# Kernel tuning notes

Measured on AMD Instinct MI355X. Metric: run time of the kernel, lower is better.

The kernel has to match this reference:

```python
import jax, jax.numpy as jnp
import numpy as np

B, S, D, H = 4, 2048, 1024, 16
DEPTH = D // H
NEG = -1000000000.0


def setup_inputs() -> dict:
    key = jax.random.key(0)
    ks = jax.random.split(key, 11)
    scale = 1.0 / np.sqrt(D)
    return {
        "q": jax.random.normal(ks[0], (B, S, D), jnp.float32),
        "k": jax.random.normal(ks[1], (B, S, D), jnp.float32),
        "v": jax.random.normal(ks[2], (B, S, D), jnp.float32),
        "wq_w": jax.random.normal(ks[3], (D, D), jnp.float32) * scale,
        "wq_b": jax.random.normal(ks[4], (D,), jnp.float32) * 0.01,
        "wk_w": jax.random.normal(ks[5], (D, D), jnp.float32) * scale,
        "wk_b": jax.random.normal(ks[6], (D,), jnp.float32) * 0.01,
        "wv_w": jax.random.normal(ks[7], (D, D), jnp.float32) * scale,
        "wv_b": jax.random.normal(ks[8], (D,), jnp.float32) * 0.01,
        "dense_w": jax.random.normal(ks[9], (D, D), jnp.float32) * scale,
        "dense_b": jax.random.normal(ks[10], (D,), jnp.float32) * 0.01,
    }


def _split_heads(x):
    # (B, S, D) -> (B, H, S, depth)
    b, s, _ = x.shape
    return x.reshape(b, s, H, DEPTH).transpose(0, 2, 1, 3)


def reference(q, k, v, wq_w, wq_b, wk_w, wk_b, wv_w, wv_b, dense_w, dense_b):
    b, s, _ = q.shape
    qh = _split_heads(q @ wq_w.T + wq_b)
    kh = _split_heads(k @ wk_w.T + wk_b)
    vh = _split_heads(v @ wv_w.T + wv_b)
    logits = jnp.einsum('bhqd,bhkd->bhqk', qh, kh) / np.sqrt(DEPTH).astype(np.float32)
    # additive causal mask (strict upper triangle = -1e9)
    mask = jnp.where(jnp.triu(jnp.ones((s, s), jnp.float32), k=1) == 1.0, NEG, 0.0)
    logits = logits + mask
    attn = jax.nn.softmax(logits, axis=-1)
    out = jnp.einsum('bhqk,bhkd->bhqd', attn, vh)
    out = out.transpose(0, 2, 1, 3).reshape(b, s, D)
    return out @ dense_w.T + dense_b
```

## Files before the change

### kernel.cpp

```cpp
#include <hip/hip_runtime.h>
#include <hip/hip_bf16.h>


typedef __attribute__((ext_vector_type(8))) short bf16x8;
typedef __attribute__((ext_vector_type(4))) float f32x4;
typedef __attribute__((ext_vector_type(8))) unsigned short u16x8;

#define MFMA16(a, b, c) __builtin_amdgcn_mfma_f32_16x16x32_bf16(a, b, c, 0, 0, 0)

#define GLOAD_LDS16(gp, lp)                                                    \
  __builtin_amdgcn_global_load_lds(                                            \
      (const __attribute__((address_space(1))) void*)(gp),                     \
      (__attribute__((address_space(3))) void*)(lp), 16, 0, 0)

__device__ __forceinline__ unsigned short f2bf(float f) {
  union { float f; unsigned u; } x; x.f = f;
  unsigned u = x.u;
  return (unsigned short)((u + 0x7fffu + ((u >> 16) & 1u)) >> 16);
}

__device__ __forceinline__ unsigned pk2(float a, float b) {
  union { __hip_bfloat162 h; unsigned u; } cv;
  cv.h = __float22bfloat162_rn(float2{a, b});
  return cv.u;
}

__global__ __launch_bounds__(256) void convert_kernel(
    const float* __restrict__ q, const float* __restrict__ k,
    const float* __restrict__ v, const float* __restrict__ wq,
    const float* __restrict__ wk, const float* __restrict__ wv,
    const float* __restrict__ wd, const float* __restrict__ bq,
    const float* __restrict__ bk, const float* __restrict__ bv,
    unsigned short* __restrict__ dst, float* __restrict__ bias_pack) {
  const size_t tid0 = (size_t)blockIdx.x * blockDim.x + threadIdx.x;
  const size_t nthreads = (size_t)gridDim.x * blockDim.x;
  if (tid0 < 3072) {
    bias_pack[tid0] = tid0 < 1024 ? bq[tid0]
                     : (tid0 < 2048 ? bk[tid0 - 1024] : bv[tid0 - 2048]);
  }
  const size_t NQ = 8192ull * 1024;
  const size_t NW = 1024ull * 1024;
  const size_t total_chunks = (3 * NQ + 4 * NW) / 8;
  for (size_t c = tid0; c < total_chunks; c += nthreads) {
    const size_t e = c * 8;
    const float* src;
    if (e < NQ) src = q + e;
    else if (e < 2 * NQ) src = k + (e - NQ);
    else if (e < 3 * NQ) src = v + (e - 2 * NQ);
    else {
      const size_t we = e - 3 * NQ;
      if (we < NW) src = wq + we;
      else if (we < 2 * NW) src = wk + (we - NW);
      else if (we < 3 * NW) src = wv + (we - 2 * NW);
      else src = wd + (we - 3 * NW);
    }
    f32x4 a = *(const f32x4*)(src);
    f32x4 b = *(const f32x4*)(src + 4);
    u16x8 o;
    o[0] = f2bf(a[0]); o[1] = f2bf(a[1]); o[2] = f2bf(a[2]); o[3] = f2bf(a[3]);
    o[4] = f2bf(b[0]); o[5] = f2bf(b[1]); o[6] = f2bf(b[2]); o[7] = f2bf(b[3]);
    *(u16x8*)(dst + e) = o;
  }
}

template <int MODE>
__global__ __launch_bounds__(256) void gemm_kernel(
    const unsigned short* __restrict__ Abase,
    const unsigned short* __restrict__ Wbase,
    const float* __restrict__ biasbase, unsigned short* __restrict__ dstb,
    float* __restrict__ dstf) {
  __shared__ __attribute__((aligned(16))) unsigned short Ablk[128 * 32];
  __shared__ __attribute__((aligned(16))) unsigned short Bblk[128 * 32];
  const size_t NQ = 8192ull * 1024, NW = 1024ull * 1024;
  int flat = ((int)blockIdx.z * 64 + blockIdx.y) * 8 + blockIdx.x;
  const int cpx = (gridDim.x * gridDim.y * gridDim.z) >> 3;
  flat = (flat & 7) * cpx + (flat >> 3);
  const int bz = flat >> 9;
  const int rem = flat & 511;
  const int by = rem >> 3, bx = rem & 7;

  const int z = bz;
  const unsigned short* A;
  const unsigned short* W;
  int m0, n0;
  if (MODE == 0 && z == 2) {
    A = Wbase + 2 * NW;
    W = Abase + 2 * NQ;
    m0 = bx * 128;
    n0 = by * 128;
  } else {
    A = Abase + (size_t)z * NQ;
    W = Wbase + (size_t)z * NW;
    m0 = by * 128;
    n0 = bx * 128;
  }
  const float* bias = biasbase + (size_t)z * 1024;
  const int tid = threadIdx.x, lane = tid & 63, w = tid >> 6;
  const int wr = (w >> 1) * 64, wc = (w & 1) * 64;
  const int llo = lane & 15, lhi = lane >> 4;
  f32x4 acc[4][4] = {};
  const unsigned short* ag = A + (size_t)(m0 + (tid >> 2)) * 1024 + (tid & 3) * 8;
  const unsigned short* wg = W + (size_t)(n0 + (tid >> 2)) * 1024 + (tid & 3) * 8;
  unsigned short* lA = &Ablk[tid * 8];
  unsigned short* lA2 = &Ablk[2048 + tid * 8];
  unsigned short* lB = &Bblk[tid * 8];
  unsigned short* lB2 = &Bblk[2048 + tid * 8];
  for (int kt = 0; kt < 32; ++kt) {
    const int ko = kt * 32;
    if (kt) __syncthreads();
    GLOAD_LDS16(ag + ko, lA);
    GLOAD_LDS16(ag + ko + 64 * 1024, lA2);
    GLOAD_LDS16(wg + ko, lB);
    GLOAD_LDS16(wg + ko + 64 * 1024, lB2);
    __syncthreads();
    bf16x8 af[4], bfr[4];
#pragma unroll
    for (int i = 0; i < 4; ++i)
      af[i] = *(const bf16x8*)&Ablk[(wr + i * 16 + llo) * 32 + lhi * 8];
#pragma unroll
    for (int i = 0; i < 4; ++i)
      bfr[i] = *(const bf16x8*)&Bblk[(wc + i * 16 + llo) * 32 + lhi * 8];
#pragma unroll
    for (int mi = 0; mi < 4; ++mi)
#pragma unroll
      for (int ni = 0; ni < 4; ++ni)
        acc[mi][ni] = MFMA16(af[mi], bfr[ni], acc[mi][ni]);
  }
  const float osc = (MODE == 0 && z == 0) ? 0.1803368801f : 1.0f;
#pragma unroll
  for (int mi = 0; mi < 4; ++mi) {
#pragma unroll
    for (int ni = 0; ni < 4; ++ni) {
      const int n = n0 + wc + ni * 16 + llo;
      const float bv = (MODE == 0) ? ((z == 2) ? 0.f : bias[n]) : bias[n];
#pragma unroll
      for (int r = 0; r < 4; ++r) {
        const int m = m0 + wr + mi * 16 + lhi * 4 + r;
        float val = acc[mi][ni][r] + bv;
        if (MODE == 1) {
          dstf[(size_t)m * 1024 + n] = val;
        } else if (z < 2) {
          val *= osc;
          const int b = m >> 11, s = m & 2047, h = n >> 6, d = n & 63;
          dstb[(size_t)z * NQ +
               (((size_t)(b * 16 + h) * 2048 + s) * 64 + d)] = f2bf(val);
        } else {
          val = acc[mi][ni][r] + bias[m];
          const int h = m >> 6, d = m & 63, b = n >> 11, sidx = n & 2047;
          const int t = sidx & 63;
          const int ps = (sidx & ~63) | ((t & 15) << 2) | (t >> 4);
          dstb[2 * NQ + (((size_t)(b * 16 + h) * 64 + d) * 2048 + ps)] = f2bf(val);
        }
      }
    }
  }
}

__global__ __launch_bounds__(256, 3) void attn_kernel(
    const unsigned short* __restrict__ Qp, const unsigned short* __restrict__ Kp,
    const unsigned short* __restrict__ Vtp, unsigned short* __restrict__ attn_out) {
  __shared__ __attribute__((aligned(16))) unsigned short Klds[2][64 * 64];
  __shared__ __attribute__((aligned(16))) unsigned short Vt[2][64 * 64];
  __shared__ __attribute__((aligned(16))) unsigned short Plds[4 * 32 * 72];
  int flat = (int)blockIdx.y * 64 + blockIdx.x;
  flat = (flat & 7) * 128 + (flat >> 3);
  const int bh = flat >> 4;
  const int qt = 15 - (flat & 15);
  const int tid = threadIdx.x, lane = tid & 63, w = tid >> 6;
  const int llo = lane & 15, lhi = lane >> 4;
  const int qbase = qt * 128 + w * 32;

  bf16x8 qf[2][2];
#pragma unroll
  for (int mi = 0; mi < 2; ++mi) {
    const unsigned short* qptr =
        Qp + ((size_t)bh * 2048 + qbase + mi * 16 + llo) * 64 + lhi * 8;
    qf[mi][0] = *(const bf16x8*)qptr;
    qf[mi][1] = *(const bf16x8*)(qptr + 32);
  }

  bf16x8 ones;
#pragma unroll
  for (int i = 0; i < 8; ++i) ones[i] = (short)0x3F80;

  f32x4 o[2][5] = {};

  const size_t kbase = (size_t)bh * (64 * 2048);
  const int r0 = tid >> 3, r1 = r0 + 32;
  const int scb = (tid & 7) * 16;
  const int kcol0 = (scb ^ ((r0 & 7) << 4)) >> 1;
  const int kcol1 = (scb ^ ((r1 & 7) << 4)) >> 1;
  const int koff0 = r0 * 64 + kcol0, koff1 = r1 * 64 + kcol1;
  const int voff0 = r0 * 2048 + kcol0, voff1 = r1 * 2048 + kcol1;
  unsigned short* pw = &Plds[w * (32 * 72)];

  const int nkt = 2 * (qt + 1);

#define STAGE(buf, kv0_)                                                       \
  do {                                                                         \
    GLOAD_LDS16(Kp + kbase + (size_t)(kv0_)*64 + koff0, &Klds[buf][tid * 8]);  \
    GLOAD_LDS16(Kp + kbase + (size_t)(kv0_)*64 + koff1,                        \
                &Klds[buf][2048 + tid * 8]);                                   \
    GLOAD_LDS16(Vtp + kbase + (kv0_) + voff0, &Vt[buf][tid * 8]);              \
    GLOAD_LDS16(Vtp + kbase + (kv0_) + voff1, &Vt[buf][2048 + tid * 8]);       \
  } while (0)

  STAGE(0, 0);
  __syncthreads();

  for (int kt = 0; kt < nkt; ++kt) {
    const int kv0 = kt * 64;
    const int cb = kt & 1;
    if (kt + 1 < nkt) STAGE(cb ^ 1, kv0 + 64);

    if (kv0 <= qbase + 31) {
      f32x4 s[2][4] = {};
      __builtin_amdgcn_s_setprio(1);
#pragma unroll
      for (int b4 = 0; b4 < 4; ++b4) {
        const int row = b4 * 16 + llo;
        const int sw = (row & 7) << 3;
        const bf16x8 k0 = *(const bf16x8*)&Klds[cb][row * 64 + ((lhi * 8) ^ sw)];
        const bf16x8 k1 =
            *(const bf16x8*)&Klds[cb][row * 64 + ((32 + lhi * 8) ^ sw)];
        s[0][b4] = MFMA16(qf[0][0], k0, s[0][b4]);
        s[0][b4] = MFMA16(qf[0][1], k1, s[0][b4]);
        s[1][b4] = MFMA16(qf[1][0], k0, s[1][b4]);
        s[1][b4] = MFMA16(qf[1][1], k1, s[1][b4]);
      }
      __builtin_amdgcn_s_setprio(0);

      const bool needm = (kv0 + 63 > qbase);
#pragma unroll
      for (int mi = 0; mi < 2; ++mi) {
#pragma unroll
        for (int r = 0; r < 4; ++r) {
          float sv0 = s[mi][0][r], sv1 = s[mi][1][r];
          float sv2 = s[mi][2][r], sv3 = s[mi][3][r];
          if (needm) {
            const int qrow = qbase + mi * 16 + lhi * 4 + r;
            if (kv0 + llo > qrow) sv0 = -1e9f;
            if (kv0 + 16 + llo > qrow) sv1 = -1e9f;
            if (kv0 + 32 + llo > qrow) sv2 = -1e9f;
            if (kv0 + 48 + llo > qrow) sv3 = -1e9f;
          }
          const float p0 = exp2f(sv0), p1 = exp2f(sv1);
          const float p2 = exp2f(sv2), p3 = exp2f(sv3);
          const int prow = mi * 16 + lhi * 4 + r;
          *(uint2*)&pw[prow * 72 + llo * 4] =
              make_uint2(pk2(p0, p1), pk2(p2, p3));
        }
      }

      bf16x8 pa[2][2];
#pragma unroll
      for (int mi = 0; mi < 2; ++mi) {
        pa[mi][0] = *(const bf16x8*)&pw[(mi * 16 + llo) * 72 + lhi * 8];
        pa[mi][1] = *(const bf16x8*)&pw[(mi * 16 + llo) * 72 + 32 + lhi * 8];
      }
      __builtin_amdgcn_s_setprio(1);
#pragma unroll
      for (int dblk = 0; dblk < 4; ++dblk) {
        const int row = dblk * 16 + llo;
        const int sw = (row & 7) << 3;
        const bf16x8 v0 = *(const bf16x8*)&Vt[cb][row * 64 + ((lhi * 8) ^ sw)];
        const bf16x8 v1 =
            *(const bf16x8*)&Vt[cb][row * 64 + ((32 + lhi * 8) ^ sw)];
        o[0][dblk] = MFMA16(pa[0][0], v0, o[0][dblk]);
        o[0][dblk] = MFMA16(pa[0][1], v1, o[0][dblk]);
        o[1][dblk] = MFMA16(pa[1][0], v0, o[1][dblk]);
        o[1][dblk] = MFMA16(pa[1][1], v1, o[1][dblk]);
      }
      o[0][4] = MFMA16(pa[0][0], ones, o[0][4]);
      o[0][4] = MFMA16(pa[0][1], ones, o[0][4]);
      o[1][4] = MFMA16(pa[1][0], ones, o[1][4]);
      o[1][4] = MFMA16(pa[1][1], ones, o[1][4]);
      __builtin_amdgcn_s_setprio(0);
    }

    __syncthreads();
  }
#undef STAGE

  const int b = bh >> 4, h = bh & 15;
#pragma unroll
  for (int mi = 0; mi < 2; ++mi) {
#pragma unroll
    for (int r = 0; r < 4; ++r) {
      const float inv = 1.0f / o[mi][4][r];
      const int qrow = qbase + mi * 16 + lhi * 4 + r;
      const size_t base = ((size_t)b * 2048 + qrow) * 1024 + h * 64;
#pragma unroll
      for (int dblk = 0; dblk < 4; ++dblk)
        attn_out[base + dblk * 16 + llo] = f2bf(o[mi][dblk][r] * inv);
    }
  }
}

extern "C" void kernel_launch(void* const* d_in, const int* in_sizes, int n_in,
                              void* d_out, int out_size, void* d_ws,
                              size_t ws_size, hipStream_t stream) {
  const float* q = (const float*)d_in[0];
  const float* k = (const float*)d_in[1];
  const float* v = (const float*)d_in[2];
  const float* wq_w = (const float*)d_in[3];
  const float* wq_b = (const float*)d_in[4];
  const float* wk_w = (const float*)d_in[5];
  const float* wk_b = (const float*)d_in[6];
  const float* wv_w = (const float*)d_in[7];
  const float* wv_b = (const float*)d_in[8];
  const float* dense_w = (const float*)d_in[9];
  const float* dense_b = (const float*)d_in[10];
  float* out = (float*)d_out;

  char* ws = (char*)d_ws;
  const size_t MB = 1024ull * 1024;
  unsigned short* qkv_bf = (unsigned short*)(ws);
  unsigned short* w_bf = (unsigned short*)(ws + 48 * MB);
  float* bias_pack = (float*)(ws + 56 * MB);
  unsigned short* qkvp = (unsigned short*)(ws + 57 * MB);
  unsigned short* attn_o = (unsigned short*)(ws + 105 * MB);
  const size_t PEL = 8192ull * 1024;

  convert_kernel<<<dim3(2048), dim3(256), 0, stream>>>(
      q, k, v, wq_w, wk_w, wv_w, dense_w, wq_b, wk_b, wv_b, qkv_bf, bias_pack);

  gemm_kernel<0><<<dim3(8, 64, 3), dim3(256), 0, stream>>>(
      qkv_bf, w_bf, bias_pack, qkvp, nullptr);

  attn_kernel<<<dim3(64, 16), dim3(256), 0, stream>>>(
      qkvp, qkvp + PEL, qkvp + 2 * PEL, attn_o);

  gemm_kernel<1><<<dim3(8, 64, 1), dim3(256), 0, stream>>>(
      attn_o, w_bf + 3ull * 1024 * 1024, dense_b, nullptr, out);
}
```

Measured before the change: 233.3 us.

## Pair causal query tiles per attention block to balance work

Each attention block now handles two 128-row query tiles, pr and 15-pr, of the same batch-head. Every block therefore does the same total causal work, and each K/V tile staged into LDS is shared by both query tiles. The grid shrinks from 1024 to 512 blocks and the launch bound drops from 3 to 2 waves per SIMD, since the doubled Q fragments and accumulators need more registers. The trade is lower occupancy and fewer blocks in exchange for balanced load and halved K/V staging.

```diff
diff --git a/kernel.cpp b/kernel.cpp
--- a/kernel.cpp
+++ b/kernel.cpp
@@ -156,34 +156,36 @@
   }
 }
 
-__global__ __launch_bounds__(256, 3) void attn_kernel(
+__global__ __launch_bounds__(256, 2) void attn_kernel(
     const unsigned short* __restrict__ Qp, const unsigned short* __restrict__ Kp,
     const unsigned short* __restrict__ Vtp, unsigned short* __restrict__ attn_out) {
   __shared__ __attribute__((aligned(16))) unsigned short Klds[2][64 * 64];
   __shared__ __attribute__((aligned(16))) unsigned short Vt[2][64 * 64];
   __shared__ __attribute__((aligned(16))) unsigned short Plds[4 * 32 * 72];
-  int flat = (int)blockIdx.y * 64 + blockIdx.x;
-  flat = (flat & 7) * 128 + (flat >> 3);
-  const int bh = flat >> 4;
-  const int qt = 15 - (flat & 15);
+  const int flat = (int)blockIdx.x;
+  const int xcd = flat & 7, idx = flat >> 3;
+  const int bh = xcd * 8 + (idx >> 3);
+  const int pr = idx & 7;
   const int tid = threadIdx.x, lane = tid & 63, w = tid >> 6;
   const int llo = lane & 15, lhi = lane >> 4;
-  const int qbase = qt * 128 + w * 32;
-
-  bf16x8 qf[2][2];
-#pragma unroll
-  for (int mi = 0; mi < 2; ++mi) {
-    const unsigned short* qptr =
-        Qp + ((size_t)bh * 2048 + qbase + mi * 16 + llo) * 64 + lhi * 8;
-    qf[mi][0] = *(const bf16x8*)qptr;
-    qf[mi][1] = *(const bf16x8*)(qptr + 32);
-  }
+  const int qbase[2] = {pr * 128 + w * 32, (15 - pr) * 128 + w * 32};
+
+  bf16x8 qf[2][2][2];
+#pragma unroll
+  for (int t = 0; t < 2; ++t)
+#pragma unroll
+    for (int mi = 0; mi < 2; ++mi) {
+      const unsigned short* qptr =
+          Qp + ((size_t)bh * 2048 + qbase[t] + mi * 16 + llo) * 64 + lhi * 8;
+      qf[t][mi][0] = *(const bf16x8*)qptr;
+      qf[t][mi][1] = *(const bf16x8*)(qptr + 32);
+    }
 
   bf16x8 ones;
 #pragma unroll
   for (int i = 0; i < 8; ++i) ones[i] = (short)0x3F80;
 
-  f32x4 o[2][5] = {};
+  f32x4 o[2][2][5] = {};
 
   const size_t kbase = (size_t)bh * (64 * 2048);
   const int r0 = tid >> 3, r1 = r0 + 32;
@@ -194,7 +196,7 @@
   const int voff0 = r0 * 2048 + kcol0, voff1 = r1 * 2048 + kcol1;
   unsigned short* pw = &Plds[w * (32 * 72)];
 
-  const int nkt = 2 * (qt + 1);
+  const int nkt = 2 * (16 - pr);
 
 #define STAGE(buf, kv0_)                                                       \
   do {                                                                         \
@@ -213,86 +215,95 @@
     const int cb = kt & 1;
     if (kt + 1 < nkt) STAGE(cb ^ 1, kv0 + 64);
 
-    if (kv0 <= qbase + 31) {
-      f32x4 s[2][4] = {};
-      __builtin_amdgcn_s_setprio(1);
-#pragma unroll
-      for (int b4 = 0; b4 < 4; ++b4) {
-        const int row = b4 * 16 + llo;
-        const int sw = (row & 7) << 3;
-        const bf16x8 k0 = *(const bf16x8*)&Klds[cb][row * 64 + ((lhi * 8) ^ sw)];
-        const bf16x8 k1 =
-            *(const bf16x8*)&Klds[cb][row * 64 + ((32 + lhi * 8) ^ sw)];
-        s[0][b4] = MFMA16(qf[0][0], k0, s[0][b4]);
-        s[0][b4] = MFMA16(qf[0][1], k1, s[0][b4]);
-        s[1][b4] = MFMA16(qf[1][0], k0, s[1][b4]);
-        s[1][b4] = MFMA16(qf[1][1], k1, s[1][b4]);
+#pragma unroll
+    for (int t = 0; t < 2; ++t) {
+      const int qb = qbase[t];
+      if (kv0 <= qb + 31) {
+        f32x4 s[2][4] = {};
+        __builtin_amdgcn_s_setprio(1);
+#pragma unroll
+        for (int b4 = 0; b4 < 4; ++b4) {
+          const int row = b4 * 16 + llo;
+          const int sw = (row & 7) << 3;
+          const bf16x8 k0 =
+              *(const bf16x8*)&Klds[cb][row * 64 + ((lhi * 8) ^ sw)];
+          const bf16x8 k1 =
+              *(const bf16x8*)&Klds[cb][row * 64 + ((32 + lhi * 8) ^ sw)];
+          s[0][b4] = MFMA16(qf[t][0][0], k0, s[0][b4]);
+          s[0][b4] = MFMA16(qf[t][0][1], k1, s[0][b4]);
+          s[1][b4] = MFMA16(qf[t][1][0], k0, s[1][b4]);
+          s[1][b4] = MFMA16(qf[t][1][1], k1, s[1][b4]);
+        }
+        __builtin_amdgcn_s_setprio(0);
+
+        const bool needm = (kv0 + 63 > qb);
+#pragma unroll
+        for (int mi = 0; mi < 2; ++mi) {
+#pragma unroll
+          for (int r = 0; r < 4; ++r) {
+            float sv0 = s[mi][0][r], sv1 = s[mi][1][r];
+            float sv2 = s[mi][2][r], sv3 = s[mi][3][r];
+            if (needm) {
+              const int qrow = qb + mi * 16 + lhi * 4 + r;
+              if (kv0 + llo > qrow) sv0 = -1e9f;
+              if (kv0 + 16 + llo > qrow) sv1 = -1e9f;
+              if (kv0 + 32 + llo > qrow) sv2 = -1e9f;
+              if (kv0 + 48 + llo > qrow) sv3 = -1e9f;
+            }
+            const float p0 = exp2f(sv0), p1 = exp2f(sv1);
+            const float p2 = exp2f(sv2), p3 = exp2f(sv3);
+            const int prow = mi * 16 + lhi * 4 + r;
+            *(uint2*)&pw[prow * 72 + llo * 4] =
+                make_uint2(pk2(p0, p1), pk2(p2, p3));
+          }
+        }
+
+        bf16x8 pa[2][2];
+#pragma unroll
+        for (int mi = 0; mi < 2; ++mi) {
+          pa[mi][0] = *(const bf16x8*)&pw[(mi * 16 + llo) * 72 + lhi * 8];
+          pa[mi][1] = *(const bf16x8*)&pw[(mi * 16 + llo) * 72 + 32 + lhi * 8];
+        }
+        __builtin_amdgcn_s_setprio(1);
+#pragma unroll
+        for (int dblk = 0; dblk < 4; ++dblk) {
+          const int row = dblk * 16 + llo;
+          const int sw = (row & 7) << 3;
+          const bf16x8 v0 =
+              *(const bf16x8*)&Vt[cb][row * 64 + ((lhi * 8) ^ sw)];
+          const bf16x8 v1 =
+              *(const bf16x8*)&Vt[cb][row * 64 + ((32 + lhi * 8) ^ sw)];
+          o[t][0][dblk] = MFMA16(pa[0][0], v0, o[t][0][dblk]);
+          o[t][0][dblk] = MFMA16(pa[0][1], v1, o[t][0][dblk]);
+          o[t][1][dblk] = MFMA16(pa[1][0], v0, o[t][1][dblk]);
+          o[t][1][dblk] = MFMA16(pa[1][1], v1, o[t][1][dblk]);
+        }
+        o[t][0][4] = MFMA16(pa[0][0], ones, o[t][0][4]);
+        o[t][0][4] = MFMA16(pa[0][1], ones, o[t][0][4]);
+        o[t][1][4] = MFMA16(pa[1][0], ones, o[t][1][4]);
+        o[t][1][4] = MFMA16(pa[1][1], ones, o[t][1][4]);
+        __builtin_amdgcn_s_setprio(0);
       }
-      __builtin_amdgcn_s_setprio(0);
-
-      const bool needm = (kv0 + 63 > qbase);
-#pragma unroll
-      for (int mi = 0; mi < 2; ++mi) {
-#pragma unroll
-        for (int r = 0; r < 4; ++r) {
-          float sv0 = s[mi][0][r], sv1 = s[mi][1][r];
-          float sv2 = s[mi][2][r], sv3 = s[mi][3][r];
-          if (needm) {
-            const int qrow = qbase + mi * 16 + lhi * 4 + r;
-            if (kv0 + llo > qrow) sv0 = -1e9f;
-            if (kv0 + 16 + llo > qrow) sv1 = -1e9f;
-            if (kv0 + 32 + llo > qrow) sv2 = -1e9f;
-            if (kv0 + 48 + llo > qrow) sv3 = -1e9f;
-          }
-          const float p0 = exp2f(sv0), p1 = exp2f(sv1);
-          const float p2 = exp2f(sv2), p3 = exp2f(sv3);
-          const int prow = mi * 16 + lhi * 4 + r;
-          *(uint2*)&pw[prow * 72 + llo * 4] =
-              make_uint2(pk2(p0, p1), pk2(p2, p3));
-        }
+    }
+
+    __syncthreads();
+  }
+#undef STAGE
+
+  const int b = bh >> 4, h = bh & 15;
+#pragma unroll
+  for (int t = 0; t < 2; ++t) {
+#pragma unroll
+    for (int mi = 0; mi < 2; ++mi) {
+#pragma unroll
+      for (int r = 0; r < 4; ++r) {
+        const float inv = 1.0f / o[t][mi][4][r];
+        const int qrow = qbase[t] + mi * 16 + lhi * 4 + r;
+        const size_t base = ((size_t)b * 2048 + qrow) * 1024 + h * 64;
+#pragma unroll
+        for (int dblk = 0; dblk < 4; ++dblk)
+          attn_out[base + dblk * 16 + llo] = f2bf(o[t][mi][dblk][r] * inv);
       }
-
-      bf16x8 pa[2][2];
-#pragma unroll
-      for (int mi = 0; mi < 2; ++mi) {
-        pa[mi][0] = *(const bf16x8*)&pw[(mi * 16 + llo) * 72 + lhi * 8];
-        pa[mi][1] = *(const bf16x8*)&pw[(mi * 16 + llo) * 72 + 32 + lhi * 8];
-      }
-      __builtin_amdgcn_s_setprio(1);
-#pragma unroll
-      for (int dblk = 0; dblk < 4; ++dblk) {
-        const int row = dblk * 16 + llo;
-        const int sw = (row & 7) << 3;
-        const bf16x8 v0 = *(const bf16x8*)&Vt[cb][row * 64 + ((lhi * 8) ^ sw)];
-        const bf16x8 v1 =
-            *(const bf16x8*)&Vt[cb][row * 64 + ((32 + lhi * 8) ^ sw)];
-        o[0][dblk] = MFMA16(pa[0][0], v0, o[0][dblk]);
-        o[0][dblk] = MFMA16(pa[0][1], v1, o[0][dblk]);
-        o[1][dblk] = MFMA16(pa[1][0], v0, o[1][dblk]);
-        o[1][dblk] = MFMA16(pa[1][1], v1, o[1][dblk]);
-      }
-      o[0][4] = MFMA16(pa[0][0], ones, o[0][4]);
-      o[0][4] = MFMA16(pa[0][1], ones, o[0][4]);
-      o[1][4] = MFMA16(pa[1][0], ones, o[1][4]);
-      o[1][4] = MFMA16(pa[1][1], ones, o[1][4]);
-      __builtin_amdgcn_s_setprio(0);
-    }
-
-    __syncthreads();
-  }
-#undef STAGE
-
-  const int b = bh >> 4, h = bh & 15;
-#pragma unroll
-  for (int mi = 0; mi < 2; ++mi) {
-#pragma unroll
-    for (int r = 0; r < 4; ++r) {
-      const float inv = 1.0f / o[mi][4][r];
-      const int qrow = qbase + mi * 16 + lhi * 4 + r;
-      const size_t base = ((size_t)b * 2048 + qrow) * 1024 + h * 64;
-#pragma unroll
-      for (int dblk = 0; dblk < 4; ++dblk)
-        attn_out[base + dblk * 16 + llo] = f2bf(o[mi][dblk][r] * inv);
     }
   }
 }
@@ -328,7 +339,7 @@
   gemm_kernel<0><<<dim3(8, 64, 3), dim3(256), 0, stream>>>(
       qkv_bf, w_bf, bias_pack, qkvp, nullptr);
 
-  attn_kernel<<<dim3(64, 16), dim3(256), 0, stream>>>(
+  attn_kernel<<<dim3(512), dim3(256), 0, stream>>>(
       qkvp, qkvp + PEL, qkvp + 2 * PEL, attn_o);
 
   gemm_kernel<1><<<dim3(8, 64, 1), dim3(256), 0, stream>>>(
```

Result: faster. 210.1 us (-9.9%).
